# Performance work log

Hardware: AMD Instinct MI355X
Metric: run time of the kernel (lower is better)

Reference implementation:

```python
import jax, jax.numpy as jnp
import numpy as np


def setup_inputs() -> dict:
    key = jax.random.key(0)
    k1, k2, k3 = jax.random.split(key, 3)
    B, N, D = 16, 512, 256
    # integer frame durations per token, 4..11 frames (avg ~7.5)
    durations = jax.random.randint(k1, (B, N), 4, 12, dtype=jnp.int32)
    # T = max over batch of total frames (static python int, mirrors torch.arange(0, max(s)))
    total_len = int(jnp.max(jnp.sum(durations, axis=-1)))
    x = jax.random.normal(k2, (B, N, D), dtype=jnp.float32)
    # positive Gaussian range (std) per token
    ranges = jax.random.uniform(k3, (B, N), minval=0.5, maxval=4.0, dtype=jnp.float32)
    return {"x": x, "durations": durations, "ranges": ranges, "total_len": total_len}


def _gaussian_weights(durations, ranges, total_len):
    # e: cumulative end frame per token, c: Gaussian center per token
    e = jnp.cumsum(durations, axis=-1).astype(jnp.float32)          # [B, N]
    c = (e - 0.5 * durations.astype(jnp.float32))[..., None]        # [B, N, 1]
    t = jnp.arange(total_len, dtype=jnp.float32)[None, None, :]     # [1, 1, T]
    inv_r2 = ranges[..., None] ** (-2)                               # [B, N, 1]
    w1 = jnp.exp(-inv_r2 * (t - c) ** 2)                             # [B, N, T]
    # original computes the exp twice (w_1 and inside w_2); same math, computed once
    w2 = jnp.sum(w1, axis=1, keepdims=True) + 1e-20                  # [B, 1, T]
    return w1 / w2


def _create_positions(durations, total_len):
    # frame-index-within-token positions: pos[b, t] = t - start_of_segment(t)
    e = jnp.cumsum(durations, axis=-1)                               # [B, N]
    starts = e - durations                                           # [B, N]
    t = jnp.arange(total_len, dtype=durations.dtype)                 # [T]
    seg = jax.vmap(lambda eb: jnp.searchsorted(eb, t, side='right'))(e)  # [B, T]
    seg = jnp.clip(seg, 0, durations.shape[-1] - 1)
    return t[None, :] - jnp.take_along_axis(starts, seg, axis=-1)    # [B, T]


def reference(x, durations, ranges, total_len):
    weights = _gaussian_weights(durations, ranges, total_len)        # [B, N, T]
    # matmul(weights.transpose(1,2), x) -> [B, T, D]
    out = jnp.einsum('bnt,bnd->btd', weights, x)
    positions = _create_positions(durations, total_len)
    return positions, out, weights
```

## Files before the change

### kernel.cpp

```cpp
#include <hip/hip_runtime.h>
#include <hip/hip_bf16.h>


#define TT  64
#define NWC 44
#define WBS 72
#define MARGIN 42.0f
#define RPB 4

typedef __attribute__((ext_vector_type(8))) short short8;
typedef __attribute__((ext_vector_type(8))) unsigned short ushort8;
typedef __attribute__((ext_vector_type(4))) float f32x4;

__device__ inline unsigned short f2bf(float f) {
    union { float f; unsigned int u; } v; v.f = f;
    unsigned int u = v.u;
    return (unsigned short)((u + 0x7FFFu + ((u >> 16) & 1u)) >> 16);
}

__global__ void scan_kernel(const int* __restrict__ dur,
                            const float* __restrict__ ranges,
                            float* __restrict__ c, float* __restrict__ ir,
                            int* __restrict__ e_i, int* __restrict__ st_i) {
    const int N = 512;
    int b = blockIdx.x, tid = threadIdx.x;
    __shared__ int sc[512];
    int d = dur[b * N + tid];
    sc[tid] = d;
    __syncthreads();
    for (int off = 1; off < 512; off <<= 1) {
        int add = (tid >= off) ? sc[tid - off] : 0;
        __syncthreads();
        sc[tid] += add;
        __syncthreads();
    }
    int e = sc[tid];
    float r = ranges[b * N + tid];
    c[b * N + tid]    = (float)e - 0.5f * (float)d;
    ir[b * N + tid]   = 1.0f / (r * r);
    e_i[b * N + tid]  = e;
    st_i[b * N + tid] = e - d;
}

__global__ __launch_bounds__(256) void pass1_kernel(
        const float* __restrict__ x, const float* __restrict__ c,
        const float* __restrict__ ir,
        const int* __restrict__ e_i, const int* __restrict__ st_i,
        float* __restrict__ pos_out ,
        float* __restrict__ out1 ,
        float* __restrict__ iw2_ws ,
        int T) {
    const int N = 512, D = 256;
    int b = blockIdx.y;
    int t0 = blockIdx.x * TT;
    int tid = threadIdx.x;

    __shared__ float c_s[512];
    __shared__ float ir_s[512];
    __shared__ int   es[512], ss[512];
    __shared__ __align__(16) unsigned short wb[TT][WBS];
    __shared__ float part[4][TT];
    __shared__ float iw2_s[TT];
    __shared__ int lohi[2];

    for (int i = tid; i < 512; i += 256) {
        c_s[i]  = c[b * N + i];
        ir_s[i] = ir[b * N + i];
        es[i]   = e_i[b * N + i];
        ss[i]   = st_i[b * N + i];
    }
    __syncthreads();

    if (tid == 0) {
        float lo_v = (float)t0 - MARGIN;
        float hi_v = (float)(t0 + TT - 1) + MARGIN;
        int lo = 0, hi = 512;
        while (lo < hi) { int m = (lo + hi) >> 1; if (c_s[m] < lo_v) lo = m + 1; else hi = m; }
        int l = lo;
        lo = 0; hi = 512;
        while (lo < hi) { int m = (lo + hi) >> 1; if (c_s[m] <= hi_v) lo = m + 1; else hi = m; }
        int h = lo - 1;
        if (h > l + NWC - 1) h = l + NWC - 1;
        lohi[0] = l; lohi[1] = h;
    }
    if (tid < TT) {
        int t = t0 + tid;
        if (t < T) {
            int lo = 0, hi = 512;
            while (lo < hi) { int m = (lo + hi) >> 1; if (es[m] <= t) lo = m + 1; else hi = m; }
            int seg = min(lo, 511);
            pos_out[b * T + t] = (float)(t - ss[seg]);
        }
    }
    __syncthreads();
    int lo_u = lohi[0], hi_u = lohi[1];

    int tl = tid & 63;
    int s  = tid >> 6;
    int t  = t0 + tl;

    float p = 0.f;
    #pragma unroll
    for (int jj = 0; jj < 16; jj++) {
        int i = s + 4 * jj;
        int n = lo_u + i;
        float w1 = 0.f;
        if (n <= hi_u && t < T) {
            float d = (float)t - c_s[n];
            w1 = expf(-ir_s[n] * d * d);
        }
        wb[tl][i] = f2bf(w1);
        p += w1;
    }
    part[s][tl] = p;
    __syncthreads();
    if (tid < TT) {
        float w2 = part[0][tid] + part[1][tid] + part[2][tid] + part[3][tid];
        float iw2 = 1.0f / (w2 + 1e-20f);
        iw2_s[tid] = iw2;
        int t2 = t0 + tid;
        if (t2 < T) iw2_ws[b * T + t2] = iw2;
    }
    __syncthreads();

    int lane = tid & 63;
    int l15  = lane & 15;
    int q    = lane >> 4;

    f32x4 acc[4][4];
    #pragma unroll
    for (int mt = 0; mt < 4; mt++)
        #pragma unroll
        for (int nt = 0; nt < 4; nt++)
            acc[mt][nt] = (f32x4){0.f, 0.f, 0.f, 0.f};

    const float* xb = x + (size_t)b * N * D;
    #pragma unroll
    for (int ks = 0; ks < 2; ks++) {
        const float* rp[8];
        #pragma unroll
        for (int j = 0; j < 8; j++) {
            int tok = lo_u + ks * 32 + q * 8 + j;
            tok = min(tok, 511);
            rp[j] = xb + (size_t)tok * D;
        }
        short8 afrag[4];
        #pragma unroll
        for (int mt = 0; mt < 4; mt++)
            afrag[mt] = *(const short8*)&wb[16 * mt + l15][ks * 32 + q * 8];
        #pragma unroll
        for (int nt = 0; nt < 4; nt++) {
            int d = 64 * s + nt * 16 + l15;
            ushort8 bu;
            #pragma unroll
            for (int j = 0; j < 8; j++) bu[j] = f2bf(rp[j][d]);
            short8 bfrag = (short8)bu;
            #pragma unroll
            for (int mt = 0; mt < 4; mt++)
                acc[mt][nt] = __builtin_amdgcn_mfma_f32_16x16x32_bf16(afrag[mt], bfrag, acc[mt][nt], 0, 0, 0);
        }
    }

    #pragma unroll
    for (int mt = 0; mt < 4; mt++) {
        #pragma unroll
        for (int r = 0; r < 4; r++) {
            int tt = t0 + 16 * mt + q * 4 + r;
            if (tt < T) {
                float iw2 = iw2_s[16 * mt + q * 4 + r];
                float* orow = out1 + ((size_t)b * T + tt) * D + 64 * s;
                #pragma unroll
                for (int nt = 0; nt < 4; nt++)
                    orow[nt * 16 + l15] = acc[mt][nt][r] * iw2;
            }
        }
    }
}

__global__ __launch_bounds__(256) void weights_kernel(
        const float* __restrict__ c, const float* __restrict__ ir,
        const float* __restrict__ iw2_ws,
        float* __restrict__ out2 , int T) {
    const int N = 512;
    int b = blockIdx.y;
    int n0 = blockIdx.x * RPB;
    int tid = threadIdx.x;
    const f32x4 z4 = (f32x4){0.f, 0.f, 0.f, 0.f};

    for (int r = 0; r < RPB; r++) {
        int n = n0 + r;
        float cn  = c[b * N + n];
        float irn = ir[b * N + n];
        float rad = 10.3f * __frsqrt_rn(irn) + 1.0f;
        int lo = (int)(cn - rad); if (lo < 0) lo = 0;
        int hi = (int)(cn + rad) + 1; if (hi > T) hi = T;

        size_t base = ((size_t)b * N + n) * (size_t)T;
        int head = (int)((4 - (base & 3)) & 3);
        if (head > T) head = T;
        if (tid < head) {
            int t = tid;
            float w = 0.f;
            if (t >= lo && t < hi) {
                float d = (float)t - cn;
                w = expf(-irn * d * d) * iw2_ws[b * T + t];
            }
            out2[base + t] = w;
        }
        int ngrp = (T - head) >> 2;
        int tail = (T - head) & 3;
        float* rowp = (float*)(out2 + base + head);
        for (int g = tid; g < ngrp; g += 256) {
            int tg = head + 4 * g;
            f32x4 v = z4;
            if (tg + 3 >= lo && tg < hi) {
                #pragma unroll
                for (int k = 0; k < 4; k++) {
                    int t = tg + k;
                    if (t >= lo && t < hi) {
                        float d = (float)t - cn;
                        v[k] = expf(-irn * d * d) * iw2_ws[b * T + t];
                    }
                }
            }
            *(f32x4*)(rowp + 4 * g) = v;
        }
        if (tid < tail) {
            int t = head + 4 * ngrp + tid;
            float w = 0.f;
            if (t >= lo && t < hi) {
                float d = (float)t - cn;
                w = expf(-irn * d * d) * iw2_ws[b * T + t];
            }
            out2[base + t] = w;
        }
    }
}

extern "C" void kernel_launch(void* const* d_in, const int* in_sizes, int n_in,
                              void* d_out, int out_size, void* d_ws, size_t ws_size,
                              hipStream_t stream) {
    const float* x      = (const float*)d_in[0];
    const int*   dur    = (const int*)d_in[1];
    const float* ranges = (const float*)d_in[2];
    const int B = 16, N = 512, D = 256;
    const int T = out_size / (B * (1 + D + N));

    float* pos_out = (float*)d_out;
    float* out1    = pos_out + (size_t)B * T;
    float* out2    = out1 + (size_t)B * T * D;

    float* c      = (float*)d_ws;
    float* ir     = c + B * N;
    int*   e_i    = (int*)(ir + B * N);
    int*   st_i   = e_i + B * N;
    float* iw2_ws = (float*)(st_i + B * N);

    scan_kernel<<<B, 512, 0, stream>>>(dur, ranges, c, ir, e_i, st_i);

    dim3 g1((T + TT - 1) / TT, B);
    pass1_kernel<<<g1, 256, 0, stream>>>(x, c, ir, e_i, st_i, pos_out, out1, iw2_ws, T);

    dim3 g2(N / RPB, B);
    weights_kernel<<<g2, 256, 0, stream>>>(c, ir, iw2_ws, out2, T);
}
```

Measured before the change: 219.7 us.

## Pre-convert x to bf16 MFMA-fragment layout and use wave-shuffle scan

Adds a transpose kernel that converts x to bf16 once and stores it in a blocked layout matching the MFMA B-fragment, so pass1 loads each fragment with one 16-byte read. Before, each lane did eight strided fp32 gathers plus conversions, and overlapping time tiles redid this work. The scan now uses wave shuffles with a small cross-wave fixup instead of a barrier-heavy shared-memory scan. The weight tile is written with vector stores, and the token window start is aligned to 8. The cost is an extra kernel launch and an extra pass over x.

```diff
diff --git a/kernel.cpp b/kernel.cpp
--- a/kernel.cpp
+++ b/kernel.cpp
@@ -18,23 +18,54 @@
     return (unsigned short)((u + 0x7FFFu + ((u >> 16) & 1u)) >> 16);
 }
 
-__global__ void scan_kernel(const int* __restrict__ dur,
-                            const float* __restrict__ ranges,
-                            float* __restrict__ c, float* __restrict__ ir,
-                            int* __restrict__ e_i, int* __restrict__ st_i) {
+__global__ __launch_bounds__(256) void xpose_kernel(
+        const float* __restrict__ x, unsigned short* __restrict__ xT) {
+    int n0 = blockIdx.x * 64, d0 = blockIdx.y * 64, b = blockIdx.z;
+    int tid = threadIdx.x;
+    __shared__ unsigned short tile[64][72];
+    const float* xb = x + ((size_t)b * 512 + n0) * 256 + d0;
+    int dl = tid & 63, ng = tid >> 6;
+    #pragma unroll
+    for (int i = 0; i < 16; i++) {
+        int nl = ng * 16 + i;
+        tile[nl][dl] = f2bf(xb[(size_t)nl * 256 + dl]);
+    }
+    __syncthreads();
+    unsigned short* xTb = xT + (size_t)b * 131072;
+    #pragma unroll
+    for (int it = 0; it < 2; it++) {
+        int ci  = it * 256 + tid;
+        int l15 = ci & 15;
+        int sub = ci >> 4;
+        int tkb = sub & 7, dkb = sub >> 3;
+        ushort8 v;
+        #pragma unroll
+        for (int k = 0; k < 8; k++) v[k] = tile[tkb * 8 + k][dkb * 16 + l15];
+        *(ushort8*)(xTb + ((((blockIdx.y * 4 + dkb) * 64) + blockIdx.x * 8 + tkb) << 7)
+                        + (l15 << 3)) = v;
+    }
+}
+
+__global__ __launch_bounds__(512) void scan_kernel(
+        const int* __restrict__ dur, const float* __restrict__ ranges,
+        float* __restrict__ c, float* __restrict__ ir,
+        int* __restrict__ e_i, int* __restrict__ st_i) {
     const int N = 512;
     int b = blockIdx.x, tid = threadIdx.x;
-    __shared__ int sc[512];
+    int lane = tid & 63, wid = tid >> 6;
     int d = dur[b * N + tid];
-    sc[tid] = d;
-    __syncthreads();
-    for (int off = 1; off < 512; off <<= 1) {
-        int add = (tid >= off) ? sc[tid - off] : 0;
-        __syncthreads();
-        sc[tid] += add;
-        __syncthreads();
-    }
-    int e = sc[tid];
+    int v = d;
+    #pragma unroll
+    for (int off = 1; off < 64; off <<= 1) {
+        int t = __shfl_up(v, off);
+        if (lane >= off) v += t;
+    }
+    __shared__ int wsum[8], woff[8];
+    if (lane == 63) wsum[wid] = v;
+    __syncthreads();
+    if (tid == 0) { int a = 0; for (int i = 0; i < 8; i++) { woff[i] = a; a += wsum[i]; } }
+    __syncthreads();
+    int e = v + woff[wid];
     float r = ranges[b * N + tid];
     c[b * N + tid]    = (float)e - 0.5f * (float)d;
     ir[b * N + tid]   = 1.0f / (r * r);
@@ -43,14 +74,15 @@
 }
 
 __global__ __launch_bounds__(256) void pass1_kernel(
-        const float* __restrict__ x, const float* __restrict__ c,
+        const unsigned short* __restrict__ xT, const float* __restrict__ c,
         const float* __restrict__ ir,
         const int* __restrict__ e_i, const int* __restrict__ st_i,
         float* __restrict__ pos_out ,
         float* __restrict__ out1 ,
         float* __restrict__ iw2_ws ,
         int T) {
-    const int N = 512, D = 256;
+    const int N = 512;
+    const int D = 256;
     int b = blockIdx.y;
     int t0 = blockIdx.x * TT;
     int tid = threadIdx.x;
@@ -81,6 +113,8 @@
         while (lo < hi) { int m = (lo + hi) >> 1; if (c_s[m] <= hi_v) lo = m + 1; else hi = m; }
         int h = lo - 1;
         if (h > l + NWC - 1) h = l + NWC - 1;
+        l &= ~7;
+        if (l > 448) l = 448;
         lohi[0] = l; lohi[1] = h;
     }
     if (tid < TT) {
@@ -99,19 +133,22 @@
     int s  = tid >> 6;
     int t  = t0 + tl;
 
+    ushort8 wv0, wv1;
     float p = 0.f;
     #pragma unroll
     for (int jj = 0; jj < 16; jj++) {
-        int i = s + 4 * jj;
-        int n = lo_u + i;
+        int n = lo_u + 16 * s + jj;
         float w1 = 0.f;
         if (n <= hi_u && t < T) {
-            float d = (float)t - c_s[n];
-            w1 = expf(-ir_s[n] * d * d);
-        }
-        wb[tl][i] = f2bf(w1);
+            float dd = (float)t - c_s[n];
+            w1 = expf(-ir_s[n] * dd * dd);
+        }
+        unsigned short hb = f2bf(w1);
+        if (jj < 8) wv0[jj] = hb; else wv1[jj - 8] = hb;
         p += w1;
     }
+    *(ushort8*)&wb[tl][16 * s]     = wv0;
+    *(ushort8*)&wb[tl][16 * s + 8] = wv1;
     part[s][tl] = p;
     __syncthreads();
     if (tid < TT) {
@@ -134,27 +171,18 @@
         for (int nt = 0; nt < 4; nt++)
             acc[mt][nt] = (f32x4){0.f, 0.f, 0.f, 0.f};
 
-    const float* xb = x + (size_t)b * N * D;
+    const unsigned short* xTb = xT + (size_t)b * 131072;
     #pragma unroll
     for (int ks = 0; ks < 2; ks++) {
-        const float* rp[8];
-        #pragma unroll
-        for (int j = 0; j < 8; j++) {
-            int tok = lo_u + ks * 32 + q * 8 + j;
-            tok = min(tok, 511);
-            rp[j] = xb + (size_t)tok * D;
-        }
+        int tokb = (lo_u >> 3) + ks * 4 + q;
         short8 afrag[4];
         #pragma unroll
         for (int mt = 0; mt < 4; mt++)
             afrag[mt] = *(const short8*)&wb[16 * mt + l15][ks * 32 + q * 8];
         #pragma unroll
         for (int nt = 0; nt < 4; nt++) {
-            int d = 64 * s + nt * 16 + l15;
-            ushort8 bu;
-            #pragma unroll
-            for (int j = 0; j < 8; j++) bu[j] = f2bf(rp[j][d]);
-            short8 bfrag = (short8)bu;
+            int dblk = 4 * s + nt;
+            short8 bfrag = *(const short8*)(xTb + (((dblk << 6) + tokb) << 7) + (l15 << 3));
             #pragma unroll
             for (int mt = 0; mt < 4; mt++)
                 acc[mt][nt] = __builtin_amdgcn_mfma_f32_16x16x32_bf16(afrag[mt], bfrag, acc[mt][nt], 0, 0, 0);
@@ -255,11 +283,16 @@
     int*   e_i    = (int*)(ir + B * N);
     int*   st_i   = e_i + B * N;
     float* iw2_ws = (float*)(st_i + B * N);
+    size_t xoff   = 4 * (size_t)(B * N) + (size_t)B * T;
+    xoff = (xoff + 7) & ~(size_t)7;
+    unsigned short* xT = (unsigned short*)((float*)d_ws + xoff);
+
+    xpose_kernel<<<dim3(8, 4, B), 256, 0, stream>>>(x, xT);
 
     scan_kernel<<<B, 512, 0, stream>>>(dur, ranges, c, ir, e_i, st_i);
 
     dim3 g1((T + TT - 1) / TT, B);
-    pass1_kernel<<<g1, 256, 0, stream>>>(x, c, ir, e_i, st_i, pos_out, out1, iw2_ws, T);
+    pass1_kernel<<<g1, 256, 0, stream>>>(xT, c, ir, e_i, st_i, pos_out, out1, iw2_ws, T);
 
     dim3 g2(N / RPB, B);
     weights_kernel<<<g2, 256, 0, stream>>>(c, ir, iw2_ws, out2, T);
```

After: 220.8 us. Within noise of the previous version (+0.5%).
